# Performance work log

Hardware: AMD Instinct MI355X
Metric: run time of the kernel (lower is better)

Reference implementation:

```python
import jax, jax.numpy as jnp
import numpy as np

N_NODES = 50000


def sage_conv(x, src, dst, Wl, bl, Wr):
    # PyG SAGEConv (aggr='mean'): out_i = Wl @ mean_{j in N(i)} x_j + bl + Wr @ x_i
    msg = x[src]                                              # [E, d] gather
    agg = jax.ops.segment_sum(msg, dst, num_segments=N_NODES)  # [N, d]
    cnt = jax.ops.segment_sum(jnp.ones((src.shape[0],), x.dtype), dst,
                              num_segments=N_NODES)
    mean = agg / jnp.maximum(cnt, 1.0)[:, None]
    return mean @ Wl.T + bl + x @ Wr.T


def graph_forward(x, edge_index, W1l, b1, W1r, W2l, b2, W2r):
    src, dst = edge_index[0], edge_index[1]
    h = jnp.tanh(sage_conv(x, src, dst, W1l, b1, W1r))
    return jnp.tanh(sage_conv(h, src, dst, W2l, b2, W2r))


def setup_inputs() -> dict:
    key = jax.random.key(0)
    ks = jax.random.split(key, 16)
    E = 800000
    IN, HID, OUT = 128, 256, 128
    s = lambda fan: 1.0 / np.sqrt(fan)
    inp = {
        'x0': jax.random.normal(ks[0], (N_NODES, IN), jnp.float32),
        'x1': jax.random.normal(ks[1], (N_NODES, IN), jnp.float32),
        'edge_index0': jax.random.randint(ks[2], (2, E), 0, N_NODES),
        'edge_index1': jax.random.randint(ks[3], (2, E), 0, N_NODES),
    }
    for g, base in ((0, 4), (1, 10)):
        inp[f'W1l_{g}'] = jax.random.normal(ks[base + 0], (HID, IN), jnp.float32) * s(IN)
        inp[f'b1_{g}'] = jnp.zeros((HID,), jnp.float32)
        inp[f'W1r_{g}'] = jax.random.normal(ks[base + 1], (HID, IN), jnp.float32) * s(IN)
        inp[f'W2l_{g}'] = jax.random.normal(ks[base + 2], (OUT, HID), jnp.float32) * s(HID)
        inp[f'b2_{g}'] = jnp.zeros((OUT,), jnp.float32)
        inp[f'W2r_{g}'] = jax.random.normal(ks[base + 3], (OUT, HID), jnp.float32) * s(HID)
    return inp


def reference(x0, x1, edge_index0, edge_index1,
              W1l_0, b1_0, W1r_0, W2l_0, b2_0, W2r_0,
              W1l_1, b1_1, W1r_1, W2l_1, b2_1, W2r_1):
    out0 = graph_forward(x0, edge_index0, W1l_0, b1_0, W1r_0, W2l_0, b2_0, W2r_0)
    out1 = graph_forward(x1, edge_index1, W1l_1, b1_1, W1r_1, W2l_1, b2_1, W2r_1)
    return jnp.concatenate([out0, out1], axis=0)
```

## Files before the change

kernel.cpp:

```cpp
#include <hip/hip_runtime.h>
#include <cstddef>

#define N_NODES 50000
#define N_EDGES 800000
#define CAP 64
#define XU (N_NODES * 16)
#define XRNG ((N_NODES + 7) / 8)

typedef __attribute__((ext_vector_type(8))) _Float16 half8;
typedef __attribute__((ext_vector_type(2))) _Float16 half2v;
typedef __attribute__((ext_vector_type(4))) float f32x4;
typedef __attribute__((ext_vector_type(4))) float f4v;

__device__ __forceinline__ float fast_tanh(float x) {
    float t = __expf(2.0f * x);
    return 1.0f - 2.0f / (t + 1.0f);
}

__global__ __launch_bounds__(256) void prep_k(
        const int* __restrict__ src0, const int* __restrict__ dst0,
        const int* __restrict__ src1, const int* __restrict__ dst1,
        int* __restrict__ cnt, int* __restrict__ adj,
        const float* __restrict__ x0, const float* __restrict__ x1,
        const float* __restrict__ w00, const float* __restrict__ w01,
        const float* __restrict__ w02, const float* __restrict__ w03,
        const float* __restrict__ w10, const float* __restrict__ w11,
        const float* __restrict__ w12, const float* __restrict__ w13,
        _Float16* __restrict__ xd, _Float16* __restrict__ wd) {
    const int triple = blockIdx.x >> 3;
    const int role3 = triple % 3;
    const int grp = blockIdx.x & 7;
    if (role3 < 2) {
        const int ftriple = (triple / 3) * 2 + role3;
        const int g = grp >> 2;
        const int lo = (grp & 3) * (2 * XRNG), hi = lo + 2 * XRNG;
        const int* src = g ? src1 : src0;
        const int* dst = g ? dst1 : dst0;
        int* cg = cnt + g * N_NODES;
        int* ag = adj + (size_t)g * N_NODES * CAP;
        for (int e = ftriple * 256 + threadIdx.x; e < N_EDGES; e += 262144) {
            int d = __builtin_nontemporal_load(dst + e);
            if (d >= lo && d < hi) {
                int sv = __builtin_nontemporal_load(src + e);
                int c = atomicAdd(&cg[d], 1);
                if (c < CAP) ag[d * CAP + c] = sv;
            }
        }
    } else {
        const int slot = (triple / 3) * 8 + grp;
        const int total = 2 * XU + 32768;
        for (int i = slot * 256 + threadIdx.x; i < total; i += 4096 * 256) {
            const float* s; _Float16* d;
            if (i < 2 * XU) {
                int g = i >= XU ? 1 : 0;
                int l = i - g * XU;
                s = (g ? x1 : x0) + (size_t)l * 8;
                d = xd + (size_t)g * ((size_t)N_NODES * 256) + (size_t)l * 8;
            } else {
                int w = i - 2 * XU;
                int g = w >> 14, m = (w >> 12) & 3, l = w & 4095;
                const float* wm;
                if (g == 0) wm = (m == 0) ? w00 : (m == 1) ? w01 : (m == 2) ? w02 : w03;
                else        wm = (m == 0) ? w10 : (m == 1) ? w11 : (m == 2) ? w12 : w13;
                s = wm + (size_t)l * 8;
                d = wd + (size_t)g * 131072 + (size_t)m * 32768 + (size_t)l * 8;
            }
            f4v v0 = __builtin_nontemporal_load((const f4v*)s);
            f4v v1 = __builtin_nontemporal_load((const f4v*)s + 1);
            half8 o;
            o[0] = (_Float16)v0[0]; o[1] = (_Float16)v0[1];
            o[2] = (_Float16)v0[2]; o[3] = (_Float16)v0[3];
            o[4] = (_Float16)v1[0]; o[5] = (_Float16)v1[1];
            o[6] = (_Float16)v1[2]; o[7] = (_Float16)v1[3];
            *(half8*)d = o;
        }
    }
}

template <int OUTM, int RSU>
__global__ __launch_bounds__(256) void gather_mean_k(
        const unsigned* __restrict__ Xu, size_t xgs,
        const int* __restrict__ cnt, const int* __restrict__ adj,
        unsigned* __restrict__ outm, size_t ogs,
        const unsigned* __restrict__ Pu, size_t pgs,
        const float* __restrict__ bias0, const float* __restrict__ bias1,
        float* __restrict__ outf, int N) {
    const int g = blockIdx.y;
    int gw = blockIdx.x * 4 + (threadIdx.x >> 6);
    if (gw >= N) return;
    const int lane = threadIdx.x & 63;
    const int deg0 = cnt[g * N_NODES + gw];
    const int deg = deg0 < CAP ? deg0 : CAP;
    const int* aj = adj + (size_t)g * N_NODES * CAP + (size_t)gw * CAP;
    const unsigned* Xl = Xu + (size_t)g * xgs + lane;
    float sx = 0.f, sy = 0.f;
    int n = 0;
    for (; n + 16 <= deg; n += 16) {
        unsigned u0  = Xl[(size_t)aj[n     ] * RSU];
        unsigned u1  = Xl[(size_t)aj[n +  1] * RSU];
        unsigned u2  = Xl[(size_t)aj[n +  2] * RSU];
        unsigned u3  = Xl[(size_t)aj[n +  3] * RSU];
        unsigned u4  = Xl[(size_t)aj[n +  4] * RSU];
        unsigned u5  = Xl[(size_t)aj[n +  5] * RSU];
        unsigned u6  = Xl[(size_t)aj[n +  6] * RSU];
        unsigned u7  = Xl[(size_t)aj[n +  7] * RSU];
        unsigned u8  = Xl[(size_t)aj[n +  8] * RSU];
        unsigned u9  = Xl[(size_t)aj[n +  9] * RSU];
        unsigned u10 = Xl[(size_t)aj[n + 10] * RSU];
        unsigned u11 = Xl[(size_t)aj[n + 11] * RSU];
        unsigned u12 = Xl[(size_t)aj[n + 12] * RSU];
        unsigned u13 = Xl[(size_t)aj[n + 13] * RSU];
        unsigned u14 = Xl[(size_t)aj[n + 14] * RSU];
        unsigned u15 = Xl[(size_t)aj[n + 15] * RSU];
        half2v h0  = __builtin_bit_cast(half2v, u0);
        half2v h1  = __builtin_bit_cast(half2v, u1);
        half2v h2  = __builtin_bit_cast(half2v, u2);
        half2v h3  = __builtin_bit_cast(half2v, u3);
        half2v h4  = __builtin_bit_cast(half2v, u4);
        half2v h5  = __builtin_bit_cast(half2v, u5);
        half2v h6  = __builtin_bit_cast(half2v, u6);
        half2v h7  = __builtin_bit_cast(half2v, u7);
        half2v h8  = __builtin_bit_cast(half2v, u8);
        half2v h9  = __builtin_bit_cast(half2v, u9);
        half2v h10 = __builtin_bit_cast(half2v, u10);
        half2v h11 = __builtin_bit_cast(half2v, u11);
        half2v h12 = __builtin_bit_cast(half2v, u12);
        half2v h13 = __builtin_bit_cast(half2v, u13);
        half2v h14 = __builtin_bit_cast(half2v, u14);
        half2v h15 = __builtin_bit_cast(half2v, u15);
        sx += (float)h0.x + (float)h1.x + (float)h2.x + (float)h3.x
            + (float)h4.x + (float)h5.x + (float)h6.x + (float)h7.x
            + (float)h8.x + (float)h9.x + (float)h10.x + (float)h11.x
            + (float)h12.x + (float)h13.x + (float)h14.x + (float)h15.x;
        sy += (float)h0.y + (float)h1.y + (float)h2.y + (float)h3.y
            + (float)h4.y + (float)h5.y + (float)h6.y + (float)h7.y
            + (float)h8.y + (float)h9.y + (float)h10.y + (float)h11.y
            + (float)h12.y + (float)h13.y + (float)h14.y + (float)h15.y;
    }
    for (; n + 4 <= deg; n += 4) {
        unsigned u0 = Xl[(size_t)aj[n    ] * RSU];
        unsigned u1 = Xl[(size_t)aj[n + 1] * RSU];
        unsigned u2 = Xl[(size_t)aj[n + 2] * RSU];
        unsigned u3 = Xl[(size_t)aj[n + 3] * RSU];
        half2v h0 = __builtin_bit_cast(half2v, u0);
        half2v h1 = __builtin_bit_cast(half2v, u1);
        half2v h2 = __builtin_bit_cast(half2v, u2);
        half2v h3 = __builtin_bit_cast(half2v, u3);
        sx += (float)h0.x + (float)h1.x + (float)h2.x + (float)h3.x;
        sy += (float)h0.y + (float)h1.y + (float)h2.y + (float)h3.y;
    }
    for (; n < deg; n++) {
        unsigned u = Xl[(size_t)aj[n] * RSU];
        half2v h = __builtin_bit_cast(half2v, u);
        sx += (float)h.x;
        sy += (float)h.y;
    }
    float inv = 1.0f / (float)(deg0 > 0 ? deg0 : 1);
    float mx = sx * inv, my = sy * inv;
    if (OUTM == 0) {
        half2v o;
        o.x = (_Float16)mx; o.y = (_Float16)my;
        outm[(size_t)g * ogs + (size_t)gw * 64 + lane] =
            __builtin_bit_cast(unsigned, o);
    } else {
        unsigned pu = Pu[(size_t)g * pgs + (size_t)gw * 64 + lane];
        half2v ph = __builtin_bit_cast(half2v, pu);
        const float* bias = g ? bias1 : bias0;
        float2 bb = ((const float2*)bias)[lane];
        float2 o;
        o.x = fast_tanh(mx + (float)ph.x + bb.x);
        o.y = fast_tanh(my + (float)ph.y + bb.y);
        ((float2*)(outf + (size_t)g * N_NODES * 128))[(size_t)gw * 64 + lane] = o;
    }
}

#define TM 128
#define TN 64
#define TK 32
#define LSTR 40
#define OSTR 72
#define SMEM_BYTES (TM * OSTR * 2)

template <bool TANH>
__global__ __launch_bounds__(256)
void gemm_f16_k(const _Float16* __restrict__ A1a, const _Float16* __restrict__ A1b,
                const _Float16* __restrict__ B1a, const _Float16* __restrict__ B1b,
                int K1,
                const _Float16* __restrict__ A2a, const _Float16* __restrict__ A2b,
                const _Float16* __restrict__ B2a, const _Float16* __restrict__ B2b,
                int K2,
                const float* __restrict__ biasa, const float* __restrict__ biasb,
                _Float16* __restrict__ outLoA, _Float16* __restrict__ outLoB,
                _Float16* __restrict__ outHiA, _Float16* __restrict__ outHiB,
                int MdLo, int MdHi, int N) {
    const int gz = blockIdx.z;
    const _Float16* A1 = gz ? A1b : A1a;
    const _Float16* B1 = gz ? B1b : B1a;
    const _Float16* A2 = gz ? A2b : A2a;
    const _Float16* B2 = gz ? B2b : B2a;
    const float* bias  = gz ? biasb : biasa;
    _Float16* outLo    = gz ? outLoB : outLoA;
    _Float16* outHi    = gz ? outHiB : outHiA;

    __shared__ char smem[SMEM_BYTES];
    _Float16 (*sA)[LSTR] = reinterpret_cast<_Float16(*)[LSTR]>(smem);
    _Float16 (*sB)[LSTR] = reinterpret_cast<_Float16(*)[LSTR]>(smem + TM * LSTR * 2);
    _Float16 (*sO)[OSTR] = reinterpret_cast<_Float16(*)[OSTR]>(smem);

    const int tid = threadIdx.x;
    const int lane = tid & 63;
    const int wave = tid >> 6;
    const int waveM = (wave & 1) * 64;
    const int waveN = (wave >> 1) * 32;
    const int rowBase = blockIdx.y * TM;
    const int colBase = blockIdx.x * TN;
    const int Ktot = K1 + K2;

    const int r0 = tid >> 2, c0 = tid & 3;
    const int r1 = r0 + 64;
    const int gr0 = rowBase + r0, gr1 = rowBase + r1;

    f32x4 acc[4][2] = {};
    half8 pA0, pA1, pB0;

    auto load_tile = [&](int k0) {
        const _Float16 *A, *B; int ko, ld;
        if (k0 < K1) { A = A1; B = B1; ko = k0;      ld = K1; }
        else         { A = A2; B = B2; ko = k0 - K1; ld = K2; }
        half8 z = {(_Float16)0, (_Float16)0, (_Float16)0, (_Float16)0,
                   (_Float16)0, (_Float16)0, (_Float16)0, (_Float16)0};
        size_t a0 = (size_t)gr0 * ld + ko + c0 * 8;
        size_t a1 = (size_t)gr1 * ld + ko + c0 * 8;
        pA0 = gr0 < N ? *(const half8*)(A + a0) : z;
        pA1 = gr1 < N ? *(const half8*)(A + a1) : z;
        pB0 = *(const half8*)(B + (size_t)(colBase + r0) * ld + ko + c0 * 8);
    };
    auto store_tile = [&]() {
        *(half8*)&sA[r0][c0 * 8] = pA0;
        *(half8*)&sA[r1][c0 * 8] = pA1;
        *(half8*)&sB[r0][c0 * 8] = pB0;
    };

    const int fm = lane & 15;
    const int fq = (lane >> 4) * 8;
    half8 fa[4], fb[2];
    auto read_frags = [&]() {
        #pragma unroll
        for (int mi = 0; mi < 4; mi++)
            fa[mi] = *(const half8*)&sA[waveM + mi * 16 + fm][fq];
        #pragma unroll
        for (int ni = 0; ni < 2; ni++)
            fb[ni] = *(const half8*)&sB[waveN + ni * 16 + fm][fq];
    };
    auto mfma_all = [&]() {
        #pragma unroll
        for (int mi = 0; mi < 4; mi++)
            #pragma unroll
            for (int ni = 0; ni < 2; ni++)
                acc[mi][ni] = __builtin_amdgcn_mfma_f32_16x16x32_f16(
                    fa[mi], fb[ni], acc[mi][ni], 0, 0, 0);
    };

    load_tile(0);
    store_tile();
    __syncthreads();

    for (int k0 = TK; k0 < Ktot; k0 += TK) {
        read_frags();
        load_tile(k0);
        mfma_all();
        __syncthreads();
        store_tile();
        __syncthreads();
    }
    read_frags();
    mfma_all();

    __syncthreads();
    {
        const int lr0 = waveM + (lane >> 4) * 4;
        const int lc0 = waveN + fm;
        #pragma unroll
        for (int ni = 0; ni < 2; ni++) {
            float bv = bias ? bias[colBase + lc0 + ni * 16] : 0.0f;
            #pragma unroll
            for (int mi = 0; mi < 4; mi++)
                #pragma unroll
                for (int r = 0; r < 4; r++) {
                    float v = acc[mi][ni][r] + bv;
                    if (TANH) v = fast_tanh(v);
                    sO[lr0 + mi * 16 + r][lc0 + ni * 16] = (_Float16)v;
                }
        }
    }
    __syncthreads();
    {
        _Float16* outp; int Md, cb;
        if (colBase < 128) { outp = outLo; Md = MdLo; cb = colBase; }
        else               { outp = outHi; Md = MdHi; cb = colBase - 128; }
        const int rr = tid >> 3;
        const int cc = (tid & 7) * 8;
        #pragma unroll
        for (int p = 0; p < 4; p++) {
            int row = p * 32 + rr;
            int grow = rowBase + row;
            if (grow < N)
                *(half8*)(outp + (size_t)grow * Md + cb + cc) =
                    *(const half8*)&sO[row][cc];
        }
    }
}

extern "C" void kernel_launch(void* const* d_in, const int* in_sizes, int n_in,
                              void* d_out, int out_size, void* d_ws, size_t ws_size,
                              hipStream_t stream) {
    const int N = N_NODES, E = N_EDGES;

    const float* x[2]   = {(const float*)d_in[0],  (const float*)d_in[1]};
    const int*   ei[2]  = {(const int*)d_in[2],    (const int*)d_in[3]};
    const float* W1l[2] = {(const float*)d_in[4],  (const float*)d_in[10]};
    const float* b1[2]  = {(const float*)d_in[5],  (const float*)d_in[11]};
    const float* W1r[2] = {(const float*)d_in[6],  (const float*)d_in[12]};
    const float* W2l[2] = {(const float*)d_in[7],  (const float*)d_in[13]};
    const float* b2[2]  = {(const float*)d_in[8],  (const float*)d_in[14]};
    const float* W2r[2] = {(const float*)d_in[9],  (const float*)d_in[15]};
    float* out = (float*)d_out;

    char* wsb = (char*)d_ws;
    const size_t MiB = 1u << 20;
    int*      cnt  = (int*)(wsb);
    int*      adj  = (int*)(wsb + 1 * MiB);
    _Float16* Wh   = (_Float16*)(wsb + 27 * MiB);
    _Float16* feat = (_Float16*)(wsb + 28 * MiB);
    _Float16* h16  = (_Float16*)(wsb + 80 * MiB);

    const size_t FGS  = (size_t)N * 256;
    const size_t WGS  = 131072;
    const size_t HSTR = (size_t)N * 256;

    const int gemm_rows = (N + TM - 1) / TM;
    const int agg_x = N / 4;

    (void)hipMemsetAsync(cnt, 0, 2 * (size_t)N * sizeof(int), stream);
    prep_k<<<12288, 256, 0, stream>>>(
        ei[0], ei[0] + E, ei[1], ei[1] + E, cnt, adj,
        x[0], x[1],
        W1l[0], W1r[0], W2l[0], W2r[0],
        W1l[1], W1r[1], W2l[1], W2r[1],
        feat, Wh);

    gather_mean_k<0, 64><<<dim3(agg_x, 2), 256, 0, stream>>>(
        (const unsigned*)feat, FGS / 2, cnt, adj,
        (unsigned*)(feat + (size_t)N * 128), FGS / 2,
        nullptr, 0, nullptr, nullptr, nullptr, N);

    _Float16* x16g[2]   = {feat, feat + FGS};
    _Float16* mean16[2] = {feat + (size_t)N * 128, feat + FGS + (size_t)N * 128};
    _Float16* z16[2]    = {feat, feat + FGS};
    _Float16* po16[2]   = {feat + (size_t)N * 128, feat + FGS + (size_t)N * 128};
    _Float16* W1l16[2]  = {Wh, Wh + WGS};
    _Float16* W1r16[2]  = {Wh + 32768, Wh + WGS + 32768};
    _Float16* W2cat[2]  = {Wh + 65536, Wh + WGS + 65536};

    if (ws_size >= (size_t)132 * MiB) {
        _Float16* h0 = h16;
        _Float16* h1 = h16 + HSTR;
        gemm_f16_k<true><<<dim3(4, gemm_rows, 2), 256, 0, stream>>>(
            mean16[0], mean16[1], W1l16[0], W1l16[1], 128,
            x16g[0], x16g[1], W1r16[0], W1r16[1], 128,
            b1[0], b1[1], h0, h1, h0 + 128, h1 + 128, 256, 256, N);
        gemm_f16_k<false><<<dim3(4, gemm_rows, 2), 256, 0, stream>>>(
            h0, h1, W2cat[0], W2cat[1], 256,
            nullptr, nullptr, nullptr, nullptr, 0,
            nullptr, nullptr, z16[0], z16[1], po16[0], po16[1], 128, 128, N);
    } else {
        for (int g = 0; g < 2; g++) {
            gemm_f16_k<true><<<dim3(4, gemm_rows, 1), 256, 0, stream>>>(
                mean16[g], mean16[g], W1l16[g], W1l16[g], 128,
                x16g[g], x16g[g], W1r16[g], W1r16[g], 128,
                b1[g], b1[g], h16, h16, h16 + 128, h16 + 128, 256, 256, N);
            gemm_f16_k<false><<<dim3(4, gemm_rows, 1), 256, 0, stream>>>(
                h16, h16, W2cat[g], W2cat[g], 256,
                nullptr, nullptr, nullptr, nullptr, 0,
                nullptr, nullptr, z16[g], z16[g], po16[g], po16[g], 128, 128, N);
        }
    }

    gather_mean_k<1, 64><<<dim3(agg_x, 2), 256, 0, stream>>>(
        (const unsigned*)feat, FGS / 2, cnt, adj,
        nullptr, 0,
        (const unsigned*)(feat + (size_t)N * 128), FGS / 2,
        b2[0], b2[1], out, N);
}
```

Before: 395.7 us.

## Overlap graph-1 gathers with graph-0 GEMMs via a fused heterogeneous kernel

Merges the gather-mean and MFMA GEMM kernels into one kernel whose blocks are assigned either a GEMM tile or a gather job, interleaving 8 gather blocks per GEMM block. The two graphs are then staggered across five launches so that one graph's memory-bound neighbor aggregation runs alongside the other graph's compute-bound GEMMs. The aim is to fill idle compute and bandwidth that sit unused when the kernels run back to back. The cost is extra launches, shared-memory allocation for every block including gather blocks (which may lower their occupancy), and runtime branching on job parameters instead of template constants.

```diff
diff --git a/kernel.cpp b/kernel.cpp
--- a/kernel.cpp
+++ b/kernel.cpp
@@ -77,41 +77,167 @@
     }
 }
 
-template <int OUTM, int RSU>
-__global__ __launch_bounds__(256) void gather_mean_k(
-        const unsigned* __restrict__ Xu, size_t xgs,
-        const int* __restrict__ cnt, const int* __restrict__ adj,
-        unsigned* __restrict__ outm, size_t ogs,
-        const unsigned* __restrict__ Pu, size_t pgs,
-        const float* __restrict__ bias0, const float* __restrict__ bias1,
-        float* __restrict__ outf, int N) {
-    const int g = blockIdx.y;
-    int gw = blockIdx.x * 4 + (threadIdx.x >> 6);
+struct GemmJob {
+    const _Float16 *A1, *B1; int K1;
+    const _Float16 *A2, *B2; int K2;
+    const float* bias; int tanhf;
+    _Float16 *outLo, *outHi; int MdLo, MdHi;
+};
+struct GatherJob {
+    const unsigned* Xu;
+    const int* cnt;
+    const int* adj;
+    unsigned* outm;
+    const unsigned* Pu;
+    const float* bias;
+    float* outf;
+    int mode;
+};
+
+#define TM 128
+#define TN 64
+#define TK 32
+#define LSTR 40
+#define OSTR 72
+#define SMEM_BYTES (TM * OSTR * 2)
+
+__device__ __forceinline__ void gemm_body(const GemmJob& J, int bx, int by,
+                                          int N, char* smem) {
+    _Float16 (*sA)[LSTR] = reinterpret_cast<_Float16(*)[LSTR]>(smem);
+    _Float16 (*sB)[LSTR] = reinterpret_cast<_Float16(*)[LSTR]>(smem + TM * LSTR * 2);
+    _Float16 (*sO)[OSTR] = reinterpret_cast<_Float16(*)[OSTR]>(smem);
+
+    const int tid = threadIdx.x;
+    const int lane = tid & 63;
+    const int wave = tid >> 6;
+    const int waveM = (wave & 1) * 64;
+    const int waveN = (wave >> 1) * 32;
+    const int rowBase = by * TM;
+    const int colBase = bx * TN;
+    const int Ktot = J.K1 + J.K2;
+
+    const int r0 = tid >> 2, c0 = tid & 3;
+    const int r1 = r0 + 64;
+    const int gr0 = rowBase + r0, gr1 = rowBase + r1;
+
+    f32x4 acc[4][2] = {};
+    half8 pA0, pA1, pB0;
+
+    auto load_tile = [&](int k0) {
+        const _Float16 *A, *B; int ko, ld;
+        if (k0 < J.K1) { A = J.A1; B = J.B1; ko = k0;        ld = J.K1; }
+        else           { A = J.A2; B = J.B2; ko = k0 - J.K1; ld = J.K2; }
+        half8 z = {(_Float16)0, (_Float16)0, (_Float16)0, (_Float16)0,
+                   (_Float16)0, (_Float16)0, (_Float16)0, (_Float16)0};
+        size_t a0 = (size_t)gr0 * ld + ko + c0 * 8;
+        size_t a1 = (size_t)gr1 * ld + ko + c0 * 8;
+        pA0 = gr0 < N ? *(const half8*)(A + a0) : z;
+        pA1 = gr1 < N ? *(const half8*)(A + a1) : z;
+        pB0 = *(const half8*)(B + (size_t)(colBase + r0) * ld + ko + c0 * 8);
+    };
+    auto store_tile = [&]() {
+        *(half8*)&sA[r0][c0 * 8] = pA0;
+        *(half8*)&sA[r1][c0 * 8] = pA1;
+        *(half8*)&sB[r0][c0 * 8] = pB0;
+    };
+
+    const int fm = lane & 15;
+    const int fq = (lane >> 4) * 8;
+    half8 fa[4], fb[2];
+    auto read_frags = [&]() {
+        #pragma unroll
+        for (int mi = 0; mi < 4; mi++)
+            fa[mi] = *(const half8*)&sA[waveM + mi * 16 + fm][fq];
+        #pragma unroll
+        for (int ni = 0; ni < 2; ni++)
+            fb[ni] = *(const half8*)&sB[waveN + ni * 16 + fm][fq];
+    };
+    auto mfma_all = [&]() {
+        #pragma unroll
+        for (int mi = 0; mi < 4; mi++)
+            #pragma unroll
+            for (int ni = 0; ni < 2; ni++)
+                acc[mi][ni] = __builtin_amdgcn_mfma_f32_16x16x32_f16(
+                    fa[mi], fb[ni], acc[mi][ni], 0, 0, 0);
+    };
+
+    load_tile(0);
+    store_tile();
+    __syncthreads();
+
+    for (int k0 = TK; k0 < Ktot; k0 += TK) {
+        read_frags();
+        load_tile(k0);
+        mfma_all();
+        __syncthreads();
+        store_tile();
+        __syncthreads();
+    }
+    read_frags();
+    mfma_all();
+
+    __syncthreads();
+    {
+        const int lr0 = waveM + (lane >> 4) * 4;
+        const int lc0 = waveN + fm;
+        #pragma unroll
+        for (int ni = 0; ni < 2; ni++) {
+            float bv = J.bias ? J.bias[colBase + lc0 + ni * 16] : 0.0f;
+            #pragma unroll
+            for (int mi = 0; mi < 4; mi++)
+                #pragma unroll
+                for (int r = 0; r < 4; r++) {
+                    float v = acc[mi][ni][r] + bv;
+                    if (J.tanhf) v = fast_tanh(v);
+                    sO[lr0 + mi * 16 + r][lc0 + ni * 16] = (_Float16)v;
+                }
+        }
+    }
+    __syncthreads();
+    {
+        _Float16* outp; int Md, cb;
+        if (colBase < 128) { outp = J.outLo; Md = J.MdLo; cb = colBase; }
+        else               { outp = J.outHi; Md = J.MdHi; cb = colBase - 128; }
+        const int rr = tid >> 3;
+        const int cc = (tid & 7) * 8;
+        #pragma unroll
+        for (int p = 0; p < 4; p++) {
+            int row = p * 32 + rr;
+            int grow = rowBase + row;
+            if (grow < N)
+                *(half8*)(outp + (size_t)grow * Md + cb + cc) =
+                    *(const half8*)&sO[row][cc];
+        }
+    }
+}
+
+__device__ __forceinline__ void gather_body(const GatherJob& J, int b, int N) {
+    int gw = b * 4 + (threadIdx.x >> 6);
     if (gw >= N) return;
     const int lane = threadIdx.x & 63;
-    const int deg0 = cnt[g * N_NODES + gw];
+    const int deg0 = J.cnt[gw];
     const int deg = deg0 < CAP ? deg0 : CAP;
-    const int* aj = adj + (size_t)g * N_NODES * CAP + (size_t)gw * CAP;
-    const unsigned* Xl = Xu + (size_t)g * xgs + lane;
+    const int* aj = J.adj + (size_t)gw * CAP;
+    const unsigned* Xl = J.Xu + lane;
     float sx = 0.f, sy = 0.f;
     int n = 0;
     for (; n + 16 <= deg; n += 16) {
-        unsigned u0  = Xl[(size_t)aj[n     ] * RSU];
-        unsigned u1  = Xl[(size_t)aj[n +  1] * RSU];
-        unsigned u2  = Xl[(size_t)aj[n +  2] * RSU];
-        unsigned u3  = Xl[(size_t)aj[n +  3] * RSU];
-        unsigned u4  = Xl[(size_t)aj[n +  4] * RSU];
-        unsigned u5  = Xl[(size_t)aj[n +  5] * RSU];
-        unsigned u6  = Xl[(size_t)aj[n +  6] * RSU];
-        unsigned u7  = Xl[(size_t)aj[n +  7] * RSU];
-        unsigned u8  = Xl[(size_t)aj[n +  8] * RSU];
-        unsigned u9  = Xl[(size_t)aj[n +  9] * RSU];
-        unsigned u10 = Xl[(size_t)aj[n + 10] * RSU];
-        unsigned u11 = Xl[(size_t)aj[n + 11] * RSU];
-        unsigned u12 = Xl[(size_t)aj[n + 12] * RSU];
-        unsigned u13 = Xl[(size_t)aj[n + 13] * RSU];
-        unsigned u14 = Xl[(size_t)aj[n + 14] * RSU];
-        unsigned u15 = Xl[(size_t)aj[n + 15] * RSU];
+        unsigned u0  = Xl[(size_t)aj[n     ] * 64];
+        unsigned u1  = Xl[(size_t)aj[n +  1] * 64];
+        unsigned u2  = Xl[(size_t)aj[n +  2] * 64];
+        unsigned u3  = Xl[(size_t)aj[n +  3] * 64];
+        unsigned u4  = Xl[(size_t)aj[n +  4] * 64];
+        unsigned u5  = Xl[(size_t)aj[n +  5] * 64];
+        unsigned u6  = Xl[(size_t)aj[n +  6] * 64];
+        unsigned u7  = Xl[(size_t)aj[n +  7] * 64];
+        unsigned u8  = Xl[(size_t)aj[n +  8] * 64];
+        unsigned u9  = Xl[(size_t)aj[n +  9] * 64];
+        unsigned u10 = Xl[(size_t)aj[n + 10] * 64];
+        unsigned u11 = Xl[(size_t)aj[n + 11] * 64];
+        unsigned u12 = Xl[(size_t)aj[n + 12] * 64];
+        unsigned u13 = Xl[(size_t)aj[n + 13] * 64];
+        unsigned u14 = Xl[(size_t)aj[n + 14] * 64];
+        unsigned u15 = Xl[(size_t)aj[n + 15] * 64];
         half2v h0  = __builtin_bit_cast(half2v, u0);
         half2v h1  = __builtin_bit_cast(half2v, u1);
         half2v h2  = __builtin_bit_cast(half2v, u2);
@@ -138,10 +264,10 @@
             + (float)h12.y + (float)h13.y + (float)h14.y + (float)h15.y;
     }
     for (; n + 4 <= deg; n += 4) {
-        unsigned u0 = Xl[(size_t)aj[n    ] * RSU];
-        unsigned u1 = Xl[(size_t)aj[n + 1] * RSU];
-        unsigned u2 = Xl[(size_t)aj[n + 2] * RSU];
-        unsigned u3 = Xl[(size_t)aj[n + 3] * RSU];
+        unsigned u0 = Xl[(size_t)aj[n    ] * 64];
+        unsigned u1 = Xl[(size_t)aj[n + 1] * 64];
+        unsigned u2 = Xl[(size_t)aj[n + 2] * 64];
+        unsigned u3 = Xl[(size_t)aj[n + 3] * 64];
         half2v h0 = __builtin_bit_cast(half2v, u0);
         half2v h1 = __builtin_bit_cast(half2v, u1);
         half2v h2 = __builtin_bit_cast(half2v, u2);
@@ -150,164 +276,50 @@
         sy += (float)h0.y + (float)h1.y + (float)h2.y + (float)h3.y;
     }
     for (; n < deg; n++) {
-        unsigned u = Xl[(size_t)aj[n] * RSU];
+        unsigned u = Xl[(size_t)aj[n] * 64];
         half2v h = __builtin_bit_cast(half2v, u);
         sx += (float)h.x;
         sy += (float)h.y;
     }
     float inv = 1.0f / (float)(deg0 > 0 ? deg0 : 1);
     float mx = sx * inv, my = sy * inv;
-    if (OUTM == 0) {
+    if (J.mode == 0) {
         half2v o;
         o.x = (_Float16)mx; o.y = (_Float16)my;
-        outm[(size_t)g * ogs + (size_t)gw * 64 + lane] =
-            __builtin_bit_cast(unsigned, o);
+        J.outm[(size_t)gw * 64 + lane] = __builtin_bit_cast(unsigned, o);
     } else {
-        unsigned pu = Pu[(size_t)g * pgs + (size_t)gw * 64 + lane];
+        unsigned pu = J.Pu[(size_t)gw * 64 + lane];
         half2v ph = __builtin_bit_cast(half2v, pu);
-        const float* bias = g ? bias1 : bias0;
-        float2 bb = ((const float2*)bias)[lane];
+        float2 bb = ((const float2*)J.bias)[lane];
         float2 o;
         o.x = fast_tanh(mx + (float)ph.x + bb.x);
         o.y = fast_tanh(my + (float)ph.y + bb.y);
-        ((float2*)(outf + (size_t)g * N_NODES * 128))[(size_t)gw * 64 + lane] = o;
-    }
-}
-
-#define TM 128
-#define TN 64
-#define TK 32
-#define LSTR 40
-#define OSTR 72
-#define SMEM_BYTES (TM * OSTR * 2)
-
-template <bool TANH>
-__global__ __launch_bounds__(256)
-void gemm_f16_k(const _Float16* __restrict__ A1a, const _Float16* __restrict__ A1b,
-                const _Float16* __restrict__ B1a, const _Float16* __restrict__ B1b,
-                int K1,
-                const _Float16* __restrict__ A2a, const _Float16* __restrict__ A2b,
-                const _Float16* __restrict__ B2a, const _Float16* __restrict__ B2b,
-                int K2,
-                const float* __restrict__ biasa, const float* __restrict__ biasb,
-                _Float16* __restrict__ outLoA, _Float16* __restrict__ outLoB,
-                _Float16* __restrict__ outHiA, _Float16* __restrict__ outHiB,
-                int MdLo, int MdHi, int N) {
-    const int gz = blockIdx.z;
-    const _Float16* A1 = gz ? A1b : A1a;
-    const _Float16* B1 = gz ? B1b : B1a;
-    const _Float16* A2 = gz ? A2b : A2a;
-    const _Float16* B2 = gz ? B2b : B2a;
-    const float* bias  = gz ? biasb : biasa;
-    _Float16* outLo    = gz ? outLoB : outLoA;
-    _Float16* outHi    = gz ? outHiB : outHiA;
-
+        ((float2*)J.outf)[(size_t)gw * 64 + lane] = o;
+    }
+}
+
+__global__ __launch_bounds__(256) void fused_k(
+        GemmJob g0, GemmJob g1, int nGemmJobs, int gemmRows,
+        GatherJob gj, int nGatherBlocks, int N) {
     __shared__ char smem[SMEM_BYTES];
-    _Float16 (*sA)[LSTR] = reinterpret_cast<_Float16(*)[LSTR]>(smem);
-    _Float16 (*sB)[LSTR] = reinterpret_cast<_Float16(*)[LSTR]>(smem + TM * LSTR * 2);
-    _Float16 (*sO)[OSTR] = reinterpret_cast<_Float16(*)[OSTR]>(smem);
-
-    const int tid = threadIdx.x;
-    const int lane = tid & 63;
-    const int wave = tid >> 6;
-    const int waveM = (wave & 1) * 64;
-    const int waveN = (wave >> 1) * 32;
-    const int rowBase = blockIdx.y * TM;
-    const int colBase = blockIdx.x * TN;
-    const int Ktot = K1 + K2;
-
-    const int r0 = tid >> 2, c0 = tid & 3;
-    const int r1 = r0 + 64;
-    const int gr0 = rowBase + r0, gr1 = rowBase + r1;
-
-    f32x4 acc[4][2] = {};
-    half8 pA0, pA1, pB0;
-
-    auto load_tile = [&](int k0) {
-        const _Float16 *A, *B; int ko, ld;
-        if (k0 < K1) { A = A1; B = B1; ko = k0;      ld = K1; }
-        else         { A = A2; B = B2; ko = k0 - K1; ld = K2; }
-        half8 z = {(_Float16)0, (_Float16)0, (_Float16)0, (_Float16)0,
-                   (_Float16)0, (_Float16)0, (_Float16)0, (_Float16)0};
-        size_t a0 = (size_t)gr0 * ld + ko + c0 * 8;
-        size_t a1 = (size_t)gr1 * ld + ko + c0 * 8;
-        pA0 = gr0 < N ? *(const half8*)(A + a0) : z;
-        pA1 = gr1 < N ? *(const half8*)(A + a1) : z;
-        pB0 = *(const half8*)(B + (size_t)(colBase + r0) * ld + ko + c0 * 8);
-    };
-    auto store_tile = [&]() {
-        *(half8*)&sA[r0][c0 * 8] = pA0;
-        *(half8*)&sA[r1][c0 * 8] = pA1;
-        *(half8*)&sB[r0][c0 * 8] = pB0;
-    };
-
-    const int fm = lane & 15;
-    const int fq = (lane >> 4) * 8;
-    half8 fa[4], fb[2];
-    auto read_frags = [&]() {
-        #pragma unroll
-        for (int mi = 0; mi < 4; mi++)
-            fa[mi] = *(const half8*)&sA[waveM + mi * 16 + fm][fq];
-        #pragma unroll
-        for (int ni = 0; ni < 2; ni++)
-            fb[ni] = *(const half8*)&sB[waveN + ni * 16 + fm][fq];
-    };
-    auto mfma_all = [&]() {
-        #pragma unroll
-        for (int mi = 0; mi < 4; mi++)
-            #pragma unroll
-            for (int ni = 0; ni < 2; ni++)
-                acc[mi][ni] = __builtin_amdgcn_mfma_f32_16x16x32_f16(
-                    fa[mi], fb[ni], acc[mi][ni], 0, 0, 0);
-    };
-
-    load_tile(0);
-    store_tile();
-    __syncthreads();
-
-    for (int k0 = TK; k0 < Ktot; k0 += TK) {
-        read_frags();
-        load_tile(k0);
-        mfma_all();
-        __syncthreads();
-        store_tile();
-        __syncthreads();
-    }
-    read_frags();
-    mfma_all();
-
-    __syncthreads();
-    {
-        const int lr0 = waveM + (lane >> 4) * 4;
-        const int lc0 = waveN + fm;
-        #pragma unroll
-        for (int ni = 0; ni < 2; ni++) {
-            float bv = bias ? bias[colBase + lc0 + ni * 16] : 0.0f;
-            #pragma unroll
-            for (int mi = 0; mi < 4; mi++)
-                #pragma unroll
-                for (int r = 0; r < 4; r++) {
-                    float v = acc[mi][ni][r] + bv;
-                    if (TANH) v = fast_tanh(v);
-                    sO[lr0 + mi * 16 + r][lc0 + ni * 16] = (_Float16)v;
-                }
-        }
-    }
-    __syncthreads();
-    {
-        _Float16* outp; int Md, cb;
-        if (colBase < 128) { outp = outLo; Md = MdLo; cb = colBase; }
-        else               { outp = outHi; Md = MdHi; cb = colBase - 128; }
-        const int rr = tid >> 3;
-        const int cc = (tid & 7) * 8;
-        #pragma unroll
-        for (int p = 0; p < 4; p++) {
-            int row = p * 32 + rr;
-            int grow = rowBase + row;
-            if (grow < N)
-                *(half8*)(outp + (size_t)grow * Md + cb + cc) =
-                    *(const half8*)&sO[row][cc];
-        }
+    const int perJob = 4 * gemmRows;
+    const int nG = nGemmJobs * perJob;
+    int gemmIdx = -1, gatherIdx = -1;
+    if (nGatherBlocks == 0) {
+        gemmIdx = blockIdx.x;
+    } else if (nG == 0) {
+        gatherIdx = blockIdx.x;
+    } else {
+        int grp9 = blockIdx.x / 9, r9 = blockIdx.x % 9;
+        if (r9 == 8) gemmIdx = grp9;
+        else         gatherIdx = grp9 * 8 + r9;
+    }
+    if (gemmIdx >= 0 && gemmIdx < nG) {
+        int j = gemmIdx / perJob;
+        int r = gemmIdx % perJob;
+        gemm_body(j ? g1 : g0, r % 4, r / 4, N, smem);
+    } else if (gatherIdx >= 0 && gatherIdx < nGatherBlocks) {
+        gather_body(gj, gatherIdx, N);
     }
 }
 
@@ -339,7 +351,8 @@
     const size_t HSTR = (size_t)N * 256;
 
     const int gemm_rows = (N + TM - 1) / TM;
-    const int agg_x = N / 4;
+    const int perJob = 4 * gemm_rows;
+    const int AGG = N / 4;
 
     (void)hipMemsetAsync(cnt, 0, 2 * (size_t)N * sizeof(int), stream);
     prep_k<<<12288, 256, 0, stream>>>(
@@ -349,46 +362,56 @@
         W1l[1], W1r[1], W2l[1], W2r[1],
         feat, Wh);
 
-    gather_mean_k<0, 64><<<dim3(agg_x, 2), 256, 0, stream>>>(
-        (const unsigned*)feat, FGS / 2, cnt, adj,
-        (unsigned*)(feat + (size_t)N * 128), FGS / 2,
-        nullptr, 0, nullptr, nullptr, nullptr, N);
-
     _Float16* x16g[2]   = {feat, feat + FGS};
     _Float16* mean16[2] = {feat + (size_t)N * 128, feat + FGS + (size_t)N * 128};
     _Float16* z16[2]    = {feat, feat + FGS};
-    _Float16* po16[2]   = {feat + (size_t)N * 128, feat + FGS + (size_t)N * 128};
+    _Float16* po16[2]   = {mean16[0], mean16[1]};
     _Float16* W1l16[2]  = {Wh, Wh + WGS};
     _Float16* W1r16[2]  = {Wh + 32768, Wh + WGS + 32768};
     _Float16* W2cat[2]  = {Wh + 65536, Wh + WGS + 65536};
 
-    if (ws_size >= (size_t)132 * MiB) {
-        _Float16* h0 = h16;
-        _Float16* h1 = h16 + HSTR;
-        gemm_f16_k<true><<<dim3(4, gemm_rows, 2), 256, 0, stream>>>(
-            mean16[0], mean16[1], W1l16[0], W1l16[1], 128,
-            x16g[0], x16g[1], W1r16[0], W1r16[1], 128,
-            b1[0], b1[1], h0, h1, h0 + 128, h1 + 128, 256, 256, N);
-        gemm_f16_k<false><<<dim3(4, gemm_rows, 2), 256, 0, stream>>>(
-            h0, h1, W2cat[0], W2cat[1], 256,
-            nullptr, nullptr, nullptr, nullptr, 0,
-            nullptr, nullptr, z16[0], z16[1], po16[0], po16[1], 128, 128, N);
+    const bool dualH = ws_size >= (size_t)132 * MiB;
+    _Float16* h0 = h16;
+    _Float16* h1 = dualH ? h16 + HSTR : h16;
+
+    GemmJob G1[2], G2[2];
+    for (int g = 0; g < 2; g++) {
+        _Float16* hg = g ? h1 : h0;
+        G1[g] = {mean16[g], W1l16[g], 128, x16g[g], W1r16[g], 128,
+                 b1[g], 1, hg, hg + 128, 256, 256};
+        G2[g] = {hg, W2cat[g], 256, nullptr, nullptr, 0,
+                 nullptr, 0, z16[g], po16[g], 128, 128};
+    }
+    GatherJob GM[2], GF[2];
+    for (int g = 0; g < 2; g++) {
+        GM[g] = {(const unsigned*)x16g[g], cnt + g * N,
+                 adj + (size_t)g * N * CAP,
+                 (unsigned*)mean16[g], nullptr, nullptr, nullptr, 0};
+        GF[g] = {(const unsigned*)z16[g], cnt + g * N,
+                 adj + (size_t)g * N * CAP,
+                 nullptr, (const unsigned*)po16[g], b2[g],
+                 out + (size_t)g * N * 128, 1};
+    }
+    GemmJob GZ = {};
+
+    if (dualH) {
+        const int mixed = perJob * 9;
+        fused_k<<<AGG, 256, 0, stream>>>(GZ, GZ, 0, gemm_rows, GM[0], AGG, N);
+        fused_k<<<mixed, 256, 0, stream>>>(G1[0], GZ, 1, gemm_rows, GM[1], AGG, N);
+        fused_k<<<2 * perJob, 256, 0, stream>>>(G2[0], G1[1], 2, gemm_rows,
+                                                GF[0], 0, N);
+        fused_k<<<mixed, 256, 0, stream>>>(G2[1], GZ, 1, gemm_rows, GF[0], AGG, N);
+        fused_k<<<AGG, 256, 0, stream>>>(GZ, GZ, 0, gemm_rows, GF[1], AGG, N);
     } else {
+        fused_k<<<AGG, 256, 0, stream>>>(GZ, GZ, 0, gemm_rows, GM[0], AGG, N);
+        fused_k<<<AGG, 256, 0, stream>>>(GZ, GZ, 0, gemm_rows, GM[1], AGG, N);
         for (int g = 0; g < 2; g++) {
-            gemm_f16_k<true><<<dim3(4, gemm_rows, 1), 256, 0, stream>>>(
-                mean16[g], mean16[g], W1l16[g], W1l16[g], 128,
-                x16g[g], x16g[g], W1r16[g], W1r16[g], 128,
-                b1[g], b1[g], h16, h16, h16 + 128, h16 + 128, 256, 256, N);
-            gemm_f16_k<false><<<dim3(4, gemm_rows, 1), 256, 0, stream>>>(
-                h16, h16, W2cat[g], W2cat[g], 256,
-                nullptr, nullptr, nullptr, nullptr, 0,
-                nullptr, nullptr, z16[g], z16[g], po16[g], po16[g], 128, 128, N);
+            fused_k<<<perJob, 256, 0, stream>>>(G1[g], GZ, 1, gemm_rows,
+                                                GF[0], 0, N);
+            fused_k<<<perJob, 256, 0, stream>>>(G2[g], GZ, 1, gemm_rows,
+                                                GF[0], 0, N);
         }
-    }
-
-    gather_mean_k<1, 64><<<dim3(agg_x, 2), 256, 0, stream>>>(
-        (const unsigned*)feat, FGS / 2, cnt, adj,
-        nullptr, 0,
-        (const unsigned*)(feat + (size_t)N * 128), FGS / 2,
-        b2[0], b2[1], out, N);
-}
+        fused_k<<<AGG, 256, 0, stream>>>(GZ, GZ, 0, gemm_rows, GF[0], AGG, N);
+        fused_k<<<AGG, 256, 0, stream>>>(GZ, GZ, 0, gemm_rows, GF[1], AGG, N);
+    }
+}
```

New measurement: 787.2 us. 1.99x slower.
